# Optimization experiments

Hardware: AMD Instinct MI355X
Metric: run time of the kernel (lower is better)

## Reference

```python
import jax, jax.numpy as jnp
import numpy as np

N_NODES = 100000
N_EDGES = 1600000
D_IN = 64
D_OUT = 64
K_PLUS = 3
ALPHA = 0.5
EXPONENT = -0.25


def _dir_norm_edge_weights(row, col, n, exponent):
    # directed_norm: D_out^exp A D_in^exp, zero-degree -> 0 weight
    ones = jnp.ones(row.shape[0], dtype=jnp.float32)
    out_deg = jax.ops.segment_sum(ones, row, num_segments=n)
    in_deg = jax.ops.segment_sum(ones, col, num_segments=n)
    out_inv = jnp.where(out_deg > 0, jnp.power(jnp.maximum(out_deg, 1.0), exponent), 0.0)
    in_inv = jnp.where(in_deg > 0, jnp.power(jnp.maximum(in_deg, 1.0), exponent), 0.0)
    return out_inv[row] * in_inv[col]


def _spmm(w, x, out_idx, gather_idx, n):
    # y[out_idx] += w * x[gather_idx]
    return jax.ops.segment_sum(w[:, None] * x[gather_idx], out_idx, num_segments=n)


def setup_inputs() -> dict:
    key = jax.random.key(0)
    ks = jax.random.split(key, 7)
    x_real = jax.random.normal(ks[0], (N_NODES, D_IN), dtype=jnp.float32)
    x_imag = jax.random.normal(ks[1], (N_NODES, D_IN), dtype=jnp.float32)
    edge_index = jax.random.randint(ks[2], (2, N_EDGES), 0, N_NODES, dtype=jnp.int32)
    s = 1.0 / np.sqrt(D_IN)
    W_real = jax.random.normal(ks[3], (K_PLUS, D_OUT, D_IN), dtype=jnp.float32) * s
    b_real = jax.random.normal(ks[4], (K_PLUS, D_OUT), dtype=jnp.float32) * s
    W_imag = jax.random.normal(ks[5], (K_PLUS, D_OUT, D_IN), dtype=jnp.float32) * s
    b_imag = jax.random.normal(ks[6], (K_PLUS, D_OUT), dtype=jnp.float32) * s
    return {"x_real": x_real, "x_imag": x_imag, "edge_index": edge_index,
            "W_real": W_real, "b_real": b_real, "W_imag": W_imag, "b_imag": b_imag}


def reference(x_real, x_imag, edge_index, W_real, b_real, W_imag, b_imag):
    n = x_real.shape[0]
    row, col = edge_index[0], edge_index[1]
    # adj_norm edge weights; adj_t_norm weights are identical scalars per edge
    # (in/out degrees swap under transpose), only the scatter direction differs.
    w = _dir_norm_edge_weights(row, col, n, EXPONENT)

    y_real = _spmm(w, x_real, row, col, n)    # adj_norm @ x_real
    y_imag = _spmm(w, x_imag, row, col, n)    # adj_norm @ x_imag
    y_real_t = _spmm(w, x_real, col, row, n)  # adj_t_norm @ x_real
    y_imag_t = _spmm(w, x_imag, col, row, n)  # adj_t_norm @ x_imag

    def lin_r(y):  # [K, N, O] per-order real linear
        return jnp.einsum('nd,kod->kno', y, W_real) + b_real[:, None, :]

    def lin_i(y):
        return jnp.einsum('nd,kod->kno', y, W_imag) + b_imag[:, None, :]

    coeffs = (0.5 ** jnp.arange(K_PLUS, dtype=jnp.float32))[:, None, None]  # exp penalty, i=0 -> 1

    lr_yr, li_yr = lin_r(y_real), lin_i(y_real)
    lr_yi, li_yi = lin_r(y_imag), lin_i(y_imag)
    lr_yrt, li_yrt = lin_r(y_real_t), lin_i(y_real_t)
    lr_yit, li_yit = lin_r(y_imag_t), lin_i(y_imag_t)

    sum_real_s2d = jnp.sum((lr_yr - li_yi) * coeffs, axis=0)
    sum_imag_s2d = jnp.sum((li_yr + lr_yi) * coeffs, axis=0)
    sum_real_d2s = jnp.sum((lr_yrt - li_yit) * coeffs, axis=0)
    # NOTE: faithful to original source, which uses y_real (not y_real_t) here.
    sum_imag_d2s = jnp.sum((li_yr + lr_yit) * coeffs, axis=0)

    total_real = ALPHA * sum_real_s2d + (1.0 - ALPHA) * sum_real_d2s
    total_imag = ALPHA * sum_imag_s2d + (1.0 - ALPHA) * sum_imag_d2s
    return total_real, total_imag
```

## Files before the change

### kernel.cpp

```cpp
#include <hip/hip_runtime.h>
#include <hip/hip_fp16.h>


constexpr int D = 64;
constexpr int GSC = 500;
constexpr int SLOTSZ = 16384;

typedef _Float16 f16x8 __attribute__((ext_vector_type(8)));
typedef float f32x4 __attribute__((ext_vector_type(4)));

__device__ __forceinline__ float2 h2_to_f2(uint p) {
  __half2 h = *(__half2*)&p;
  return __half22float2(h);
}

__global__ __launch_bounds__(1024) void prep_kernel(
    const float* __restrict__ Wr, const float* __restrict__ br,
    const float* __restrict__ Wi, const float* __restrict__ bi,
    uint4* __restrict__ Bfrag, float* __restrict__ cR, float* __restrict__ cI,
    int* __restrict__ Ccur, int NBUK) {
  __shared__ uint sWh[4096];
  int t = threadIdx.x;
  for (int i = t; i < 4096; i += 1024) {
    int o = i >> 6, d = i & 63;
    float wr = Wr[i] + 0.5f * Wr[4096 + i] + 0.25f * Wr[8192 + i];
    float wi = Wi[i] + 0.5f * Wi[4096 + i] + 0.25f * Wi[8192 + i];
    __half2 h = __floats2half2_rn(wr, wi);
    sWh[d * 64 + o] = *(uint*)&h;
  }
  if (t < 64) {
    float brv = br[t] + 0.5f * br[64 + t] + 0.25f * br[128 + t];
    float biv = bi[t] + 0.5f * bi[64 + t] + 0.25f * bi[128 + t];
    cR[t] = brv - biv;
    cI[t] = brv + biv;
  }
  for (int i = t; i < 2 * NBUK; i += 1024) Ccur[i << 4] = (i % NBUK) * SLOTSZ;
  __syncthreads();
  for (int tt = t; tt < 2048; tt += 1024) {
    int ln = tt & 63, fr = tt >> 6;
    int mat = fr >> 4, kt = (fr >> 2) & 3, nt = fr & 3;
    int o = (ln & 15) + 16 * nt;
    int k0 = 8 * (ln >> 4) + 32 * kt;
    uint wbits[4];
#pragma unroll
    for (int jj = 0; jj < 4; ++jj) {
      float vv[2];
#pragma unroll
      for (int s = 0; s < 2; ++s) {
        int k = k0 + 2 * jj + s;
        float2 wrwi = h2_to_f2(sWh[(k & 63) * 64 + o]);
        vv[s] = (k < 64) ? wrwi.x : (mat ? wrwi.y : -wrwi.y);
      }
      __half2 hh = __floats2half2_rn(vv[0], vv[1]);
      wbits[jj] = *(uint*)&hh;
    }
    Bfrag[tt] = make_uint4(wbits[0], wbits[1], wbits[2], wbits[3]);
  }
}

__global__ __launch_bounds__(256) void part_scatter(
    const int* __restrict__ row, const int* __restrict__ col,
    int* __restrict__ Ccur,
    uint* __restrict__ pout, uint* __restrict__ pin, int E, int NBUK, int CH) {
  __shared__ int co[256], ci[256];
  int t = threadIdx.x, g = blockIdx.x;
  co[t] = 0;
  ci[t] = 0;
  __syncthreads();
  int e0 = g * CH, e1 = min(E, e0 + CH);
  int g0 = e0 >> 2, g1 = (e1 + 3) >> 2;
  for (int gi = g0 + t; gi < g1; gi += 256) {
    int4 r4 = ((const int4*)row)[gi];
    int4 c4 = ((const int4*)col)[gi];
    atomicAdd(&co[r4.x >> 9], 1);
    atomicAdd(&co[r4.y >> 9], 1);
    atomicAdd(&co[r4.z >> 9], 1);
    atomicAdd(&co[r4.w >> 9], 1);
    atomicAdd(&ci[c4.x >> 9], 1);
    atomicAdd(&ci[c4.y >> 9], 1);
    atomicAdd(&ci[c4.z >> 9], 1);
    atomicAdd(&ci[c4.w >> 9], 1);
  }
  __syncthreads();
  if (t < NBUK) {
    int c = co[t];
    co[t] = c ? atomicAdd(&Ccur[t << 4], c) : 0;
    c = ci[t];
    ci[t] = c ? atomicAdd(&Ccur[(NBUK + t) << 4], c) : 0;
  }
  __syncthreads();
  for (int gi = g0 + t; gi < g1; gi += 256) {
    int4 r4 = ((const int4*)row)[gi];
    int4 c4 = ((const int4*)col)[gi];
#define SCAT1(R, C)                                          \
  {                                                          \
    int po = atomicAdd(&co[(R) >> 9], 1);                    \
    pout[po] = ((uint)((R) & 511) << 17) | (uint)(C);        \
    int pi = atomicAdd(&ci[(C) >> 9], 1);                    \
    pin[pi] = ((uint)((C) & 511) << 17) | (uint)(R);         \
  }
    SCAT1(r4.x, c4.x);
    SCAT1(r4.y, c4.y);
    SCAT1(r4.z, c4.z);
    SCAT1(r4.w, c4.w);
#undef SCAT1
  }
}

__global__ __launch_bounds__(256) void offsets_kernel(
    const uint* __restrict__ pout, const uint* __restrict__ pin,
    const int* __restrict__ Ccur,
    int2* __restrict__ ofsp_out, int2* __restrict__ ofsp_in,
    float* __restrict__ inv_out, float* __restrict__ inv_in,
    int NBUK, int N) {
  const uint* p = blockIdx.y ? pin : pout;
  int2* ofsp = blockIdx.y ? ofsp_in : ofsp_out;
  float* inv = blockIdx.y ? inv_in : inv_out;
  __shared__ int ld[512];
  __shared__ int ws[4];
  int t = threadIdx.x, b = blockIdx.x;
  ld[t] = 0;
  ld[t + 256] = 0;
  __syncthreads();
  int win_s = b * SLOTSZ;
  int win_e = Ccur[((blockIdx.y ? NBUK : 0) + b) << 4];
  int j = win_s + t;
  for (; j + 768 < win_e; j += 1024) {
    uint p0 = p[j], p1 = p[j + 256], p2 = p[j + 512], p3 = p[j + 768];
    atomicAdd(&ld[p0 >> 17], 1);
    atomicAdd(&ld[p1 >> 17], 1);
    atomicAdd(&ld[p2 >> 17], 1);
    atomicAdd(&ld[p3 >> 17], 1);
  }
  for (; j < win_e; j += 256) atomicAdd(&ld[p[j] >> 17], 1);
  __syncthreads();
  int a0 = ld[2 * t], a1 = ld[2 * t + 1], sm = a0 + a1;
  int lane = t & 63, wv = t >> 6, sc = sm;
#pragma unroll
  for (int off = 1; off < 64; off <<= 1) {
    int u = __shfl_up(sc, off);
    if (lane >= off) sc += u;
  }
  if (lane == 63) ws[wv] = sc;
  __syncthreads();
  int wbase = 0;
#pragma unroll
  for (int w = 0; w < 4; ++w)
    if (w < wv) wbase += ws[w];
  int excl = wbase + sc - sm;
  int n0 = (b << 9) + 2 * t;
  int st0 = win_s + excl;
  if (n0 < N) {
    ofsp[n0] = make_int2(st0, st0 + a0);
    inv[n0] = a0 ? rsqrtf(sqrtf((float)a0)) : 0.0f;
  }
  if (n0 + 1 < N) {
    ofsp[n0 + 1] = make_int2(st0 + a0, st0 + a0 + a1);
    inv[n0 + 1] = a1 ? rsqrtf(sqrtf((float)a1)) : 0.0f;
  }
}

__global__ __launch_bounds__(256) void bucket_fill(
    const uint* __restrict__ pout, const uint* __restrict__ pin,
    const int* __restrict__ Ccur,
    const int2* __restrict__ ofsp_out, const int2* __restrict__ ofsp_in,
    const float* __restrict__ inv_out, const float* __restrict__ inv_in,
    uint* __restrict__ idx_out, uint* __restrict__ idx_in, int NBUK, int N) {
  const uint* p = blockIdx.y ? pin : pout;
  const int2* ofsp = blockIdx.y ? ofsp_in : ofsp_out;
  const float* invnb = blockIdx.y ? inv_out : inv_in;
  uint* idx = blockIdx.y ? idx_in : idx_out;
  __shared__ int cur[512];
  int t = threadIdx.x, b = blockIdx.x;
  int n0 = (b << 9) + t;
  cur[t] = (n0 < N) ? ofsp[n0].x : 0;
  cur[t + 256] = (n0 + 256 < N) ? ofsp[n0 + 256].x : 0;
  __syncthreads();
  int s = b * SLOTSZ;
  int e = Ccur[((blockIdx.y ? NBUK : 0) + b) << 4];
#define FILL1(PK)                                                       \
  {                                                                     \
    uint nbr = (PK) & 0x1FFFFu;                                         \
    uint hb = (uint)__half_as_ushort(__float2half(invnb[nbr]));         \
    int pos = atomicAdd(&cur[(PK) >> 17], 1);                           \
    idx[pos] = (hb << 17) | nbr;                                        \
  }
  int j = s + t;
  for (; j + 768 < e; j += 1024) {
    uint p0 = p[j], p1 = p[j + 256], p2 = p[j + 512], p3 = p[j + 768];
    FILL1(p0);
    FILL1(p1);
    FILL1(p2);
    FILL1(p3);
  }
  for (; j < e; j += 256) {
    uint pk = p[j];
    FILL1(pk);
  }
#undef FILL1
}


__global__ void pack_kernel(const float* __restrict__ xr, const float* __restrict__ xi,
                            uint* __restrict__ xp, int total4) {
  int i = blockIdx.x * blockDim.x + threadIdx.x;
  if (i < total4) {
    float4 a = ((const float4*)xr)[i];
    float4 b = ((const float4*)xi)[i];
    __half2 h;
    uint4 o;
    h = __floats2half2_rn(a.x, b.x); o.x = *(uint*)&h;
    h = __floats2half2_rn(a.y, b.y); o.y = *(uint*)&h;
    h = __floats2half2_rn(a.z, b.z); o.z = *(uint*)&h;
    h = __floats2half2_rn(a.w, b.w); o.w = *(uint*)&h;
    ((uint4*)xp)[i] = o;
  }
}

__global__ __launch_bounds__(256) void gather_kernel(
    const uint4* __restrict__ xp4,
    const uint* __restrict__ idx_out, const uint* __restrict__ idx_in,
    const int2* __restrict__ ofsp_out, const int2* __restrict__ ofsp_in,
    const float* __restrict__ inv_out, const float* __restrict__ inv_in,
    uint* __restrict__ Apack, int N) {
  int wv = threadIdx.x >> 6;
  int lane = threadIdx.x & 63;
  int sub = lane >> 4;
  int q = lane & 15;
  int wid = blockIdx.x * 4 + wv;
  int nw = gridDim.x * 4;
  for (int n = wid; n < N; n += nw) {
    float4 u1 = {0, 0, 0, 0}, s1 = {0, 0, 0, 0};
    float4 v2 = {0, 0, 0, 0}, s2 = {0, 0, 0, 0};
#define ACC(P, SC, U, S)                                                \
  {                                                                     \
    float2 a0 = h2_to_f2((P).x), a1 = h2_to_f2((P).y);                  \
    float2 a2 = h2_to_f2((P).z), a3 = h2_to_f2((P).w);                  \
    U.x += SC * a0.x; S.x += SC * a0.y; U.y += SC * a1.x; S.y += SC * a1.y; \
    U.z += SC * a2.x; S.z += SC * a2.y; U.w += SC * a3.x; S.w += SC * a3.y; \
  }
#define DEC(E) __half2float(__ushort_as_half((ushort)((E) >> 17)))
    {
      int2 se = ofsp_out[n];
      int lo = se.x, hi = se.y;
      int len8 = (hi - lo) & ~7;
      int j = lo;
      for (; j < lo + len8; j += 8) {
        uint e0 = idx_out[j + sub];
        uint e1 = idx_out[j + 4 + sub];
        uint4 p0 = xp4[(size_t)(e0 & 0x1FFFFu) * 16 + q];
        uint4 p1 = xp4[(size_t)(e1 & 0x1FFFFu) * 16 + q];
        float sc0 = DEC(e0), sc1 = DEC(e1);
        ACC(p0, sc0, u1, s1);
        ACC(p1, sc1, u1, s1);
      }
      for (; j < hi; j += 4) {
        if (j + sub < hi) {
          uint e0 = idx_out[j + sub];
          uint4 p0 = xp4[(size_t)(e0 & 0x1FFFFu) * 16 + q];
          float sc0 = DEC(e0);
          ACC(p0, sc0, u1, s1);
        }
      }
    }
    {
      int2 se = ofsp_in[n];
      int lo = se.x, hi = se.y;
      int len8 = (hi - lo) & ~7;
      int j = lo;
      for (; j < lo + len8; j += 8) {
        uint e0 = idx_in[j + sub];
        uint e1 = idx_in[j + 4 + sub];
        uint4 p0 = xp4[(size_t)(e0 & 0x1FFFFu) * 16 + q];
        uint4 p1 = xp4[(size_t)(e1 & 0x1FFFFu) * 16 + q];
        float sc0 = DEC(e0), sc1 = DEC(e1);
        ACC(p0, sc0, v2, s2);
        ACC(p1, sc1, v2, s2);
      }
      for (; j < hi; j += 4) {
        if (j + sub < hi) {
          uint e0 = idx_in[j + sub];
          uint4 p0 = xp4[(size_t)(e0 & 0x1FFFFu) * 16 + q];
          float sc0 = DEC(e0);
          ACC(p0, sc0, v2, s2);
        }
      }
    }
#undef ACC
#undef DEC
#pragma unroll
    for (int m = 16; m < 64; m <<= 1) {
      u1.x += __shfl_xor(u1.x, m); u1.y += __shfl_xor(u1.y, m);
      u1.z += __shfl_xor(u1.z, m); u1.w += __shfl_xor(u1.w, m);
      s1.x += __shfl_xor(s1.x, m); s1.y += __shfl_xor(s1.y, m);
      s1.z += __shfl_xor(s1.z, m); s1.w += __shfl_xor(s1.w, m);
      v2.x += __shfl_xor(v2.x, m); v2.y += __shfl_xor(v2.y, m);
      v2.z += __shfl_xor(v2.z, m); v2.w += __shfl_xor(v2.w, m);
      s2.x += __shfl_xor(s2.x, m); s2.y += __shfl_xor(s2.y, m);
      s2.z += __shfl_xor(s2.z, m); s2.w += __shfl_xor(s2.w, m);
    }
    if (sub == 0) {
      float io = inv_out[n], ii = inv_in[n];
      float4 uu = make_float4(io * u1.x, io * u1.y, io * u1.z, io * u1.w);
      float4 vv = make_float4(ii * v2.x, ii * v2.y, ii * v2.z, ii * v2.w);
      float4 ss = make_float4(io * s1.x + ii * s2.x, io * s1.y + ii * s2.y,
                              io * s1.z + ii * s2.z, io * s1.w + ii * s2.w);
      uint* base = Apack + (size_t)n * 96 + 2 * q;
      __half2 h;
      uint2 w;
      h = __floats2half2_rn(0.5f * (uu.x + vv.x), 0.5f * (uu.y + vv.y)); w.x = *(uint*)&h;
      h = __floats2half2_rn(0.5f * (uu.z + vv.z), 0.5f * (uu.w + vv.w)); w.y = *(uint*)&h;
      *(uint2*)base = w;
      h = __floats2half2_rn(0.5f * ss.x, 0.5f * ss.y); w.x = *(uint*)&h;
      h = __floats2half2_rn(0.5f * ss.z, 0.5f * ss.w); w.y = *(uint*)&h;
      *(uint2*)(base + 32) = w;
      h = __floats2half2_rn(uu.x, uu.y); w.x = *(uint*)&h;
      h = __floats2half2_rn(uu.z, uu.w); w.y = *(uint*)&h;
      *(uint2*)(base + 64) = w;
    }
  }
}

__global__ __launch_bounds__(256) void gemm_kernel(
    const ushort* __restrict__ Apack, const uint4* __restrict__ Bfrag,
    const float* __restrict__ cR, const float* __restrict__ cI,
    float* __restrict__ out_real, float* __restrict__ out_imag, int N) {
  __shared__ uint4 sB[2048];
  for (int i = threadIdx.x; i < 2048; i += 256) sB[i] = Bfrag[i];
  __syncthreads();
  int lane = threadIdx.x & 63, wv = threadIdx.x >> 6;
  int l15 = lane & 15, l4 = lane >> 4;
  float bR[4], bI[4];
#pragma unroll
  for (int nt = 0; nt < 4; ++nt) {
    bR[nt] = cR[l15 + 16 * nt];
    bI[nt] = cI[l15 + 16 * nt];
  }
  int tiles = (N + 15) >> 4;
  int gw = blockIdx.x * 4 + wv, nw = gridDim.x * 4;
  for (int tt = gw; tt < tiles; tt += nw) {
    int n0 = tt << 4;
    int arow = min(n0 + l15, N - 1);
    const ushort* ap = Apack + (size_t)arow * 192 + 8 * l4;
    f16x8 a[6];
#pragma unroll
    for (int kt = 0; kt < 6; ++kt) a[kt] = *(const f16x8*)(ap + 32 * kt);
    f32x4 cr[4], ci[4];
#pragma unroll
    for (int nt = 0; nt < 4; ++nt) {
      cr[nt] = (f32x4){0.f, 0.f, 0.f, 0.f};
      ci[nt] = (f32x4){0.f, 0.f, 0.f, 0.f};
    }
#pragma unroll
    for (int kt = 0; kt < 4; ++kt) {
#pragma unroll
      for (int nt = 0; nt < 4; ++nt) {
        f16x8 b0 = *(const f16x8*)&sB[(kt * 4 + nt) * 64 + lane];
        cr[nt] = __builtin_amdgcn_mfma_f32_16x16x32_f16(a[kt], b0, cr[nt], 0, 0, 0);
        f16x8 b1 = *(const f16x8*)&sB[(16 + kt * 4 + nt) * 64 + lane];
        ci[nt] = __builtin_amdgcn_mfma_f32_16x16x32_f16(a[kt + 2], b1, ci[nt], 0, 0, 0);
      }
    }
#pragma unroll
    for (int nt = 0; nt < 4; ++nt) {
#pragma unroll
      for (int r = 0; r < 4; ++r) {
        int node = n0 + 4 * l4 + r;
        if (node < N) {
          out_real[(size_t)node * 64 + l15 + 16 * nt] = cr[nt][r] + bR[nt];
          out_imag[(size_t)node * 64 + l15 + 16 * nt] = ci[nt][r] + bI[nt];
        }
      }
    }
  }
}

extern "C" void kernel_launch(void* const* d_in, const int* in_sizes, int n_in,
                              void* d_out, int out_size, void* d_ws, size_t ws_size,
                              hipStream_t stream) {
  const float* x_real = (const float*)d_in[0];
  const float* x_imag = (const float*)d_in[1];
  const int* edge = (const int*)d_in[2];
  const float* W_real = (const float*)d_in[3];
  const float* b_real = (const float*)d_in[4];
  const float* W_imag = (const float*)d_in[5];
  const float* b_imag = (const float*)d_in[6];

  const int N = in_sizes[0] / D;
  const int E = in_sizes[2] / 2;
  const int* row = edge;
  const int* col = edge + E;

  const int NBUK = (N + 511) >> 9;
  const int CH = ((E / GSC + 3) & ~3);
  const size_t SLOTS = (size_t)NBUK * SLOTSZ;

  uint* xp       = (uint*)d_ws;
  uint* idx_out  = xp + (size_t)N * D;
  uint* idx_in   = idx_out + SLOTS;
  uint* Apack    = idx_in + SLOTS;
  uint* pout     = Apack;
  uint* pin      = pout + SLOTS;
  uint4* Bfrag   = (uint4*)(Apack + (size_t)N * 96);
  int* Ccur      = (int*)(Bfrag + 2048);
  int2* ofsp_out = (int2*)(Ccur + 2 * NBUK * 16);
  int2* ofsp_in  = ofsp_out + N;
  float* inv_out = (float*)(ofsp_in + N);
  float* inv_in  = inv_out + N;
  float* cR      = inv_in + N;
  float* cI      = cR + 64;

  float* out_real = (float*)d_out;
  float* out_imag = out_real + (size_t)N * D;

  prep_kernel<<<1, 1024, 0, stream>>>(W_real, b_real, W_imag, b_imag,
                                      Bfrag, cR, cI, Ccur, NBUK);

  pack_kernel<<<(N * 16 + 255) / 256, 256, 0, stream>>>(x_real, x_imag, xp, N * 16);

  part_scatter<<<GSC, 256, 0, stream>>>(row, col, Ccur, pout, pin, E, NBUK, CH);

  offsets_kernel<<<dim3(NBUK, 2), 256, 0, stream>>>(pout, pin, Ccur,
                                                    ofsp_out, ofsp_in,
                                                    inv_out, inv_in, NBUK, N);

  bucket_fill<<<dim3(NBUK, 2), 256, 0, stream>>>(pout, pin, Ccur,
                                                 ofsp_out, ofsp_in,
                                                 inv_out, inv_in,
                                                 idx_out, idx_in, NBUK, N);

  gather_kernel<<<4096, 256, 0, stream>>>((const uint4*)xp, idx_out, idx_in,
                                          ofsp_out, ofsp_in, inv_out, inv_in,
                                          Apack, N);
  gemm_kernel<<<1568, 256, 0, stream>>>((const ushort*)Apack, Bfrag, cR, cI,
                                        out_real, out_imag, N);
}
```

Baseline: 325.0 us.

## Fuse CSR offset and fill kernels with 256-node buckets, gather degree scales directly

Halves the bucket size to 256 nodes (8192 slots) so one 256-thread block can compute per-node offsets and then fill the CSR index in the same kernel, merging offsets_kernel and bucket_fill into build_kernel. The neighbor scale is no longer packed as fp16 into the index word; the gather kernel reads inv_in/inv_out per edge instead. This removes one launch and the per-edge fp16 scale lookup at build time, but adds an extra random 4-byte load per edge in the gather. It also doubles the number of buckets and the partition atomics on the Ccur counters.

```diff
diff --git a/kernel.cpp b/kernel.cpp
--- a/kernel.cpp
+++ b/kernel.cpp
@@ -4,7 +4,7 @@
 
 constexpr int D = 64;
 constexpr int GSC = 500;
-constexpr int SLOTSZ = 16384;
+constexpr int SLOTSZ = 8192;
 
 typedef _Float16 f16x8 __attribute__((ext_vector_type(8)));
 typedef float f32x4 __attribute__((ext_vector_type(4)));
@@ -34,7 +34,10 @@
     cR[t] = brv - biv;
     cI[t] = brv + biv;
   }
-  for (int i = t; i < 2 * NBUK; i += 1024) Ccur[i << 4] = (i % NBUK) * SLOTSZ;
+  for (int i = t; i < 2 * NBUK; i += 1024) {
+    int b = (i < NBUK) ? i : (i - NBUK);
+    Ccur[i << 4] = b * SLOTSZ;
+  }
   __syncthreads();
   for (int tt = t; tt < 2048; tt += 1024) {
     int ln = tt & 63, fr = tt >> 6;
@@ -62,31 +65,33 @@
     const int* __restrict__ row, const int* __restrict__ col,
     int* __restrict__ Ccur,
     uint* __restrict__ pout, uint* __restrict__ pin, int E, int NBUK, int CH) {
-  __shared__ int co[256], ci[256];
+  __shared__ int co[512], ci[512];
   int t = threadIdx.x, g = blockIdx.x;
   co[t] = 0;
+  co[t + 256] = 0;
   ci[t] = 0;
+  ci[t + 256] = 0;
   __syncthreads();
   int e0 = g * CH, e1 = min(E, e0 + CH);
   int g0 = e0 >> 2, g1 = (e1 + 3) >> 2;
   for (int gi = g0 + t; gi < g1; gi += 256) {
     int4 r4 = ((const int4*)row)[gi];
     int4 c4 = ((const int4*)col)[gi];
-    atomicAdd(&co[r4.x >> 9], 1);
-    atomicAdd(&co[r4.y >> 9], 1);
-    atomicAdd(&co[r4.z >> 9], 1);
-    atomicAdd(&co[r4.w >> 9], 1);
-    atomicAdd(&ci[c4.x >> 9], 1);
-    atomicAdd(&ci[c4.y >> 9], 1);
-    atomicAdd(&ci[c4.z >> 9], 1);
-    atomicAdd(&ci[c4.w >> 9], 1);
-  }
-  __syncthreads();
-  if (t < NBUK) {
-    int c = co[t];
-    co[t] = c ? atomicAdd(&Ccur[t << 4], c) : 0;
-    c = ci[t];
-    ci[t] = c ? atomicAdd(&Ccur[(NBUK + t) << 4], c) : 0;
+    atomicAdd(&co[r4.x >> 8], 1);
+    atomicAdd(&co[r4.y >> 8], 1);
+    atomicAdd(&co[r4.z >> 8], 1);
+    atomicAdd(&co[r4.w >> 8], 1);
+    atomicAdd(&ci[c4.x >> 8], 1);
+    atomicAdd(&ci[c4.y >> 8], 1);
+    atomicAdd(&ci[c4.z >> 8], 1);
+    atomicAdd(&ci[c4.w >> 8], 1);
+  }
+  __syncthreads();
+  for (int i = t; i < NBUK; i += 256) {
+    int c = co[i];
+    co[i] = c ? atomicAdd(&Ccur[i << 4], c) : 0;
+    c = ci[i];
+    ci[i] = c ? atomicAdd(&Ccur[(NBUK + i) << 4], c) : 0;
   }
   __syncthreads();
   for (int gi = g0 + t; gi < g1; gi += 256) {
@@ -94,10 +99,10 @@
     int4 c4 = ((const int4*)col)[gi];
 #define SCAT1(R, C)                                          \
   {                                                          \
-    int po = atomicAdd(&co[(R) >> 9], 1);                    \
-    pout[po] = ((uint)((R) & 511) << 17) | (uint)(C);        \
-    int pi = atomicAdd(&ci[(C) >> 9], 1);                    \
-    pin[pi] = ((uint)((C) & 511) << 17) | (uint)(R);         \
+    int po = atomicAdd(&co[(R) >> 8], 1);                    \
+    pout[po] = ((uint)((R) & 255) << 17) | (uint)(C);        \
+    int pi = atomicAdd(&ci[(C) >> 8], 1);                    \
+    pin[pi] = ((uint)((C) & 255) << 17) | (uint)(R);         \
   }
     SCAT1(r4.x, c4.x);
     SCAT1(r4.y, c4.y);
@@ -107,35 +112,35 @@
   }
 }
 
-__global__ __launch_bounds__(256) void offsets_kernel(
+__global__ __launch_bounds__(256) void build_kernel(
     const uint* __restrict__ pout, const uint* __restrict__ pin,
     const int* __restrict__ Ccur,
     int2* __restrict__ ofsp_out, int2* __restrict__ ofsp_in,
     float* __restrict__ inv_out, float* __restrict__ inv_in,
-    int NBUK, int N) {
+    uint* __restrict__ idx_out, uint* __restrict__ idx_in, int NBUK, int N) {
   const uint* p = blockIdx.y ? pin : pout;
   int2* ofsp = blockIdx.y ? ofsp_in : ofsp_out;
   float* inv = blockIdx.y ? inv_in : inv_out;
-  __shared__ int ld[512];
+  uint* idx = blockIdx.y ? idx_in : idx_out;
+  __shared__ int ld[256], cur[256];
   __shared__ int ws[4];
   int t = threadIdx.x, b = blockIdx.x;
   ld[t] = 0;
-  ld[t + 256] = 0;
-  __syncthreads();
-  int win_s = b * SLOTSZ;
-  int win_e = Ccur[((blockIdx.y ? NBUK : 0) + b) << 4];
-  int j = win_s + t;
-  for (; j + 768 < win_e; j += 1024) {
+  __syncthreads();
+  int s = b * SLOTSZ;
+  int e = Ccur[((blockIdx.y ? NBUK : 0) + b) << 4];
+  int j = s + t;
+  for (; j + 768 < e; j += 1024) {
     uint p0 = p[j], p1 = p[j + 256], p2 = p[j + 512], p3 = p[j + 768];
     atomicAdd(&ld[p0 >> 17], 1);
     atomicAdd(&ld[p1 >> 17], 1);
     atomicAdd(&ld[p2 >> 17], 1);
     atomicAdd(&ld[p3 >> 17], 1);
   }
-  for (; j < win_e; j += 256) atomicAdd(&ld[p[j] >> 17], 1);
-  __syncthreads();
-  int a0 = ld[2 * t], a1 = ld[2 * t + 1], sm = a0 + a1;
-  int lane = t & 63, wv = t >> 6, sc = sm;
+  for (; j < e; j += 256) atomicAdd(&ld[p[j] >> 17], 1);
+  __syncthreads();
+  int d = ld[t];
+  int lane = t & 63, wv = t >> 6, sc = d;
 #pragma unroll
   for (int off = 1; off < 64; off <<= 1) {
     int u = __shfl_up(sc, off);
@@ -147,45 +152,20 @@
 #pragma unroll
   for (int w = 0; w < 4; ++w)
     if (w < wv) wbase += ws[w];
-  int excl = wbase + sc - sm;
-  int n0 = (b << 9) + 2 * t;
-  int st0 = win_s + excl;
-  if (n0 < N) {
-    ofsp[n0] = make_int2(st0, st0 + a0);
-    inv[n0] = a0 ? rsqrtf(sqrtf((float)a0)) : 0.0f;
-  }
-  if (n0 + 1 < N) {
-    ofsp[n0 + 1] = make_int2(st0 + a0, st0 + a0 + a1);
-    inv[n0 + 1] = a1 ? rsqrtf(sqrtf((float)a1)) : 0.0f;
-  }
-}
-
-__global__ __launch_bounds__(256) void bucket_fill(
-    const uint* __restrict__ pout, const uint* __restrict__ pin,
-    const int* __restrict__ Ccur,
-    const int2* __restrict__ ofsp_out, const int2* __restrict__ ofsp_in,
-    const float* __restrict__ inv_out, const float* __restrict__ inv_in,
-    uint* __restrict__ idx_out, uint* __restrict__ idx_in, int NBUK, int N) {
-  const uint* p = blockIdx.y ? pin : pout;
-  const int2* ofsp = blockIdx.y ? ofsp_in : ofsp_out;
-  const float* invnb = blockIdx.y ? inv_out : inv_in;
-  uint* idx = blockIdx.y ? idx_in : idx_out;
-  __shared__ int cur[512];
-  int t = threadIdx.x, b = blockIdx.x;
-  int n0 = (b << 9) + t;
-  cur[t] = (n0 < N) ? ofsp[n0].x : 0;
-  cur[t + 256] = (n0 + 256 < N) ? ofsp[n0 + 256].x : 0;
-  __syncthreads();
-  int s = b * SLOTSZ;
-  int e = Ccur[((blockIdx.y ? NBUK : 0) + b) << 4];
-#define FILL1(PK)                                                       \
-  {                                                                     \
-    uint nbr = (PK) & 0x1FFFFu;                                         \
-    uint hb = (uint)__half_as_ushort(__float2half(invnb[nbr]));         \
-    int pos = atomicAdd(&cur[(PK) >> 17], 1);                           \
-    idx[pos] = (hb << 17) | nbr;                                        \
-  }
-  int j = s + t;
+  int start = s + wbase + sc - d;
+  cur[t] = start;
+  int n = (b << 8) + t;
+  if (n < N) {
+    ofsp[n] = make_int2(start, start + d);
+    inv[n] = d ? rsqrtf(sqrtf((float)d)) : 0.0f;
+  }
+  __syncthreads();
+  j = s + t;
+#define FILL1(PK)                                  \
+  {                                                \
+    int pos = atomicAdd(&cur[(PK) >> 17], 1);      \
+    idx[pos] = (PK) & 0x1FFFFu;                    \
+  }
   for (; j + 768 < e; j += 1024) {
     uint p0 = p[j], p1 = p[j + 256], p2 = p[j + 512], p3 = p[j + 768];
     FILL1(p0);
@@ -239,7 +219,6 @@
     U.x += SC * a0.x; S.x += SC * a0.y; U.y += SC * a1.x; S.y += SC * a1.y; \
     U.z += SC * a2.x; S.z += SC * a2.y; U.w += SC * a3.x; S.w += SC * a3.y; \
   }
-#define DEC(E) __half2float(__ushort_as_half((ushort)((E) >> 17)))
     {
       int2 se = ofsp_out[n];
       int lo = se.x, hi = se.y;
@@ -248,17 +227,17 @@
       for (; j < lo + len8; j += 8) {
         uint e0 = idx_out[j + sub];
         uint e1 = idx_out[j + 4 + sub];
-        uint4 p0 = xp4[(size_t)(e0 & 0x1FFFFu) * 16 + q];
-        uint4 p1 = xp4[(size_t)(e1 & 0x1FFFFu) * 16 + q];
-        float sc0 = DEC(e0), sc1 = DEC(e1);
+        uint4 p0 = xp4[(size_t)e0 * 16 + q];
+        uint4 p1 = xp4[(size_t)e1 * 16 + q];
+        float sc0 = inv_in[e0], sc1 = inv_in[e1];
         ACC(p0, sc0, u1, s1);
         ACC(p1, sc1, u1, s1);
       }
       for (; j < hi; j += 4) {
         if (j + sub < hi) {
           uint e0 = idx_out[j + sub];
-          uint4 p0 = xp4[(size_t)(e0 & 0x1FFFFu) * 16 + q];
-          float sc0 = DEC(e0);
+          uint4 p0 = xp4[(size_t)e0 * 16 + q];
+          float sc0 = inv_in[e0];
           ACC(p0, sc0, u1, s1);
         }
       }
@@ -271,23 +250,22 @@
       for (; j < lo + len8; j += 8) {
         uint e0 = idx_in[j + sub];
         uint e1 = idx_in[j + 4 + sub];
-        uint4 p0 = xp4[(size_t)(e0 & 0x1FFFFu) * 16 + q];
-        uint4 p1 = xp4[(size_t)(e1 & 0x1FFFFu) * 16 + q];
-        float sc0 = DEC(e0), sc1 = DEC(e1);
+        uint4 p0 = xp4[(size_t)e0 * 16 + q];
+        uint4 p1 = xp4[(size_t)e1 * 16 + q];
+        float sc0 = inv_out[e0], sc1 = inv_out[e1];
         ACC(p0, sc0, v2, s2);
         ACC(p1, sc1, v2, s2);
       }
       for (; j < hi; j += 4) {
         if (j + sub < hi) {
           uint e0 = idx_in[j + sub];
-          uint4 p0 = xp4[(size_t)(e0 & 0x1FFFFu) * 16 + q];
-          float sc0 = DEC(e0);
+          uint4 p0 = xp4[(size_t)e0 * 16 + q];
+          float sc0 = inv_out[e0];
           ACC(p0, sc0, v2, s2);
         }
       }
     }
 #undef ACC
-#undef DEC
 #pragma unroll
     for (int m = 16; m < 64; m <<= 1) {
       u1.x += __shfl_xor(u1.x, m); u1.y += __shfl_xor(u1.y, m);
@@ -391,7 +369,7 @@
   const int* row = edge;
   const int* col = edge + E;
 
-  const int NBUK = (N + 511) >> 9;
+  const int NBUK = (N + 255) >> 8;
   const int CH = ((E / GSC + 3) & ~3);
   const size_t SLOTS = (size_t)NBUK * SLOTSZ;
 
@@ -420,14 +398,10 @@
 
   part_scatter<<<GSC, 256, 0, stream>>>(row, col, Ccur, pout, pin, E, NBUK, CH);
 
-  offsets_kernel<<<dim3(NBUK, 2), 256, 0, stream>>>(pout, pin, Ccur,
-                                                    ofsp_out, ofsp_in,
-                                                    inv_out, inv_in, NBUK, N);
-
-  bucket_fill<<<dim3(NBUK, 2), 256, 0, stream>>>(pout, pin, Ccur,
-                                                 ofsp_out, ofsp_in,
-                                                 inv_out, inv_in,
-                                                 idx_out, idx_in, NBUK, N);
+  build_kernel<<<dim3(NBUK, 2), 256, 0, stream>>>(pout, pin, Ccur,
+                                                  ofsp_out, ofsp_in,
+                                                  inv_out, inv_in,
+                                                  idx_out, idx_in, NBUK, N);
 
   gather_kernel<<<4096, 256, 0, stream>>>((const uint4*)xp, idx_out, idx_in,
                                           ofsp_out, ofsp_in, inv_out, inv_in,
```

New measurement: 331.3 us. About the same (+2.0%).
